# Kernel optimization log

Measured on AMD Instinct MI355X. Metric: run time of the kernel, lower is better.

Reference implementation:

```python
import jax, jax.numpy as jnp
import numpy as np

N_NODES = 50000
N_EDGES = 800000
C_IN = 128
C_OUT = 128
K = 6


def setup_inputs() -> dict:
    key = jax.random.key(0)
    ks = jax.random.split(key, 8)
    nodes = jax.random.normal(ks[0], (N_NODES, C_IN), dtype=jnp.float32)
    edges = jax.random.uniform(ks[1], (N_EDGES,), dtype=jnp.float32)
    senders = jax.random.randint(ks[2], (N_EDGES,), 0, N_NODES, dtype=jnp.int32)
    receivers = jax.random.randint(ks[3], (N_EDGES,), 0, N_NODES, dtype=jnp.int32)
    # K independent Dense(out_channels) layers (kernel + bias each), plus extra module bias
    W = jax.random.normal(ks[4], (K, C_IN, C_OUT), dtype=jnp.float32) / jnp.sqrt(jnp.float32(C_IN))
    b_dense = jax.random.normal(ks[5], (K, C_OUT), dtype=jnp.float32) * 0.01
    bias = jnp.zeros((C_OUT,), dtype=jnp.float32)
    return {"nodes": nodes, "edges": edges, "senders": senders, "receivers": receivers,
            "W": W, "b_dense": b_dense, "bias": bias}


def reference(nodes, edges, senders, receivers, W, b_dense, bias):
    n = nodes.shape[0]
    # Laplacian L = D - A with A[s, r] = w. deg_i = sum of weights of edges with sender i.
    deg = jax.ops.segment_sum(edges, senders, num_segments=n)
    # lambda_max = 2 * max(L.data) where L.data = concat(deg, -edges)
    lambda_max = 2.0 * jnp.maximum(deg.max(), (-edges).max())
    scale = 2.0 / lambda_max  # L_hat = (2/lambda_max) * L

    def Lmatvec(x):  # (2L/lambda_max) @ x via gather + segment_sum
        agg = jax.ops.segment_sum(edges[:, None] * x[receivers], senders, num_segments=n)
        return scale * (deg[:, None] * x - agg)

    Tx0 = nodes
    out = Tx0 @ W[0] + b_dense[0]
    Tx1 = Lmatvec(Tx0)
    out = out + Tx1 @ W[1] + b_dense[1]
    for k in range(2, K):
        Tx2 = 2.0 * Lmatvec(Tx1) - Tx0
        out = out + Tx2 @ W[k] + b_dense[k]
        Tx0, Tx1 = Tx1, Tx2
    return out + bias
```

## Files before the change

### kernel.cpp

```cpp
#include <hip/hip_runtime.h>
#include <hip/hip_fp16.h>

#define C 128
#define KORD 6
#define KD (KORD * C)
#define EPB 2048

typedef __attribute__((ext_vector_type(8))) short short8;
typedef __attribute__((ext_vector_type(4))) float f32x4;

__device__ __forceinline__ short f2bf(float f) {
  unsigned u = __float_as_uint(f);
  unsigned r = (u + 0x7fffu + ((u >> 16) & 1u)) >> 16;
  return (short)r;
}
__device__ __forceinline__ float bf2f(short s) {
  return __uint_as_float(((unsigned)(unsigned short)s) << 16);
}

__device__ __forceinline__ unsigned enc_f32(float f) {
  unsigned u = __float_as_uint(f);
  return (u & 0x80000000u) ? ~u : (u | 0x80000000u);
}
__device__ __forceinline__ float dec_f32(unsigned u) {
  return (u & 0x80000000u) ? __uint_as_float(u ^ 0x80000000u) : __uint_as_float(~u);
}

__global__ void prep_kernel(const float* __restrict__ W, const float* __restrict__ bd,
                            const float* __restrict__ bias, short* __restrict__ Wt,
                            float* __restrict__ bsum, const float* __restrict__ nodes,
                            short* __restrict__ xb, int n) {
  int i = blockIdx.x * blockDim.x + threadIdx.x;
  if (i < KD * C) {
    int k = i >> 7, nn = i & 127;
    Wt[(size_t)nn * KD + k] = f2bf(W[i]);
  }
  if (i < C) {
    float s = bias[i];
#pragma unroll
    for (int k = 0; k < KORD; ++k) s += bd[k * C + i];
    bsum[i] = s;
  }
  if (i < n * 32) {
    int row = i >> 5, c4 = i & 31;
    float4 v = ((const float4*)nodes)[(size_t)row * 32 + c4];
    short4 o;
    o.x = f2bf(v.x); o.y = f2bf(v.y); o.z = f2bf(v.z); o.w = f2bf(v.w);
    ((short4*)(xb + (size_t)row * KD))[c4] = o;
  }
}

__global__ __launch_bounds__(256) void p1_count_kernel(const int* __restrict__ senders,
                                                       const float* __restrict__ edges, int ne,
                                                       int* __restrict__ hist, int NB,
                                                       unsigned* __restrict__ umax) {
  __shared__ int h[256];
  int t = threadIdx.x;
  h[t] = 0;
  __syncthreads();
  int base = blockIdx.x * EPB;
  int end = min(base + EPB, ne);
  float m = -INFINITY;
  for (int i = base + t; i < end; i += 256) {
    atomicAdd(&h[senders[i] >> 8], 1);
    m = fmaxf(m, -edges[i]);
  }
#pragma unroll
  for (int off = 32; off > 0; off >>= 1) m = fmaxf(m, __shfl_down(m, off, 64));
  if ((t & 63) == 0) atomicMax(umax, enc_f32(m));
  __syncthreads();
  hist[t * NB + blockIdx.x] = h[t];
}

__global__ __launch_bounds__(1024) void scan1_kernel(const int* __restrict__ counts,
                                                     int* __restrict__ offsets,
                                                     int* __restrict__ bsums, int n) {
  int t = threadIdx.x;
  int i = blockIdx.x * 1024 + t;
  int lane = t & 63, w = t >> 6;
  int v = (i < n) ? counts[i] : 0;
  int s = v;
#pragma unroll
  for (int d = 1; d < 64; d <<= 1) {
    int o = __shfl_up(s, d, 64);
    if (lane >= d) s += o;
  }
  __shared__ int wsum[16];
  if (lane == 63) wsum[w] = s;
  __syncthreads();
  if (t < 16) {
    int ws = wsum[t];
#pragma unroll
    for (int d = 1; d < 16; d <<= 1) {
      int o = __shfl_up(ws, d, 64);
      if (t >= d) ws += o;
    }
    wsum[t] = ws;
  }
  __syncthreads();
  int excl = s - v + (w > 0 ? wsum[w - 1] : 0);
  if (i < n) offsets[i] = excl;
  if (t == 1023) bsums[blockIdx.x] = wsum[15];
}

__global__ __launch_bounds__(1024) void scan2_kernel(int* __restrict__ bsums, int nb) {
  int t = threadIdx.x;
  int lane = t & 63, w = t >> 6;
  int v = (t < nb) ? bsums[t] : 0;
  int s = v;
#pragma unroll
  for (int d = 1; d < 64; d <<= 1) {
    int o = __shfl_up(s, d, 64);
    if (lane >= d) s += o;
  }
  __shared__ int wsum[16];
  if (lane == 63) wsum[w] = s;
  __syncthreads();
  if (t < 16) {
    int ws = wsum[t];
#pragma unroll
    for (int d = 1; d < 16; d <<= 1) {
      int o = __shfl_up(ws, d, 64);
      if (t >= d) ws += o;
    }
    wsum[t] = ws;
  }
  __syncthreads();
  int excl = s - v + (w > 0 ? wsum[w - 1] : 0);
  if (t < nb) bsums[t] = excl;
}

__global__ __launch_bounds__(256) void p1_scatter_kernel(
    const int* __restrict__ senders, const int* __restrict__ receivers,
    const float* __restrict__ edges, int ne, const int* __restrict__ scanned,
    const int* __restrict__ bsums, int NB, int2* __restrict__ bkt) {
  __shared__ int basec[256];
  int t = threadIdx.x;
  int idx = t * NB + blockIdx.x;
  basec[t] = scanned[idx] + bsums[idx >> 10];
  __syncthreads();
  int base = blockIdx.x * EPB;
  int end = min(base + EPB, ne);
  for (int i = base + t; i < end; i += 256) {
    int s = senders[i];
    int pos = atomicAdd(&basec[s >> 8], 1);
    int2 rec;
    rec.x = __float_as_int(edges[i]);
    rec.y = receivers[i] | ((s & 255) << 16);
    bkt[pos] = rec;
  }
}

__global__ __launch_bounds__(256) void p2_finalize_kernel(
    const int2* __restrict__ bkt, const int* __restrict__ scanned,
    const int* __restrict__ bsums, int NB, int NBUCK, int ne, int n,
    unsigned* __restrict__ csr_wr, int* __restrict__ offsets, float* __restrict__ degf,
    unsigned* __restrict__ umax, int* __restrict__ ticket, float* __restrict__ scalep) {
  __shared__ int h[256];
  __shared__ int cur[256];
  __shared__ float dg[256];
  __shared__ int wsum[4];
  __shared__ float wmax[4];
  int t = threadIdx.x;
  int b = blockIdx.x;
  int i0 = b * NB;
  int base = scanned[i0] + bsums[i0 >> 10];
  int bend = ne;
  if (b != NBUCK - 1) {
    int i1 = (b + 1) * NB;
    bend = scanned[i1] + bsums[i1 >> 10];
  }
  h[t] = 0;
  dg[t] = 0.f;
  __syncthreads();
  for (int i = base + t; i < bend; i += 256) atomicAdd(&h[(bkt[i].y >> 16) & 255], 1);
  __syncthreads();
  int lane = t & 63, w = t >> 6;
  int v = h[t];
  int s = v;
#pragma unroll
  for (int d = 1; d < 64; d <<= 1) {
    int o = __shfl_up(s, d, 64);
    if (lane >= d) s += o;
  }
  if (lane == 63) wsum[w] = s;
  __syncthreads();
  int carry = 0;
#pragma unroll
  for (int j = 0; j < 4; ++j) carry += (j < w) ? wsum[j] : 0;
  int excl = s - v + carry;
  int node = b * 256 + t;
  if (node < n) offsets[node] = base + excl;
  cur[t] = base + excl;
  __syncthreads();
  for (int i = base + t; i < bend; i += 256) {
    int2 rec = bkt[i];
    int bin = (rec.y >> 16) & 255;
    int pos = atomicAdd(&cur[bin], 1);
    __half hh = __float2half(__int_as_float(rec.x));
    csr_wr[pos] = (unsigned)(rec.y & 0xFFFF) | ((unsigned)__half_as_ushort(hh) << 16);
    atomicAdd(&dg[bin], __half2float(hh));
  }
  __syncthreads();
  float d = dg[t];
  if (node < n) degf[node] = d;
  float m = (node < n) ? d : 0.f;
#pragma unroll
  for (int off = 32; off > 0; off >>= 1) m = fmaxf(m, __shfl_down(m, off, 64));
  if (lane == 0) wmax[w] = m;
  __syncthreads();
  if (t == 0) {
    float mm = fmaxf(fmaxf(wmax[0], wmax[1]), fmaxf(wmax[2], wmax[3]));
    atomicMax(umax, enc_f32(mm));
    if (b == NBUCK - 1) offsets[n] = ne;
    __threadfence();
    int done = atomicAdd(ticket, 1);
    if (done == NBUCK - 1) {
      unsigned cu = atomicMax(umax, 0u);
      scalep[0] = 1.0f / dec_f32(cu);
    }
  }
}

__global__ __launch_bounds__(256, 8) void matvec_kernel(
    const short* __restrict__ xg,
    const short* __restrict__ zg,
    short* __restrict__ yg,
    const float* __restrict__ deg, const int* __restrict__ offsets,
    const unsigned* __restrict__ csr_wr, const float* __restrict__ scalep, float coef, int n) {
  int wid = (blockIdx.x * blockDim.x + threadIdx.x) >> 6;
  int lane = threadIdx.x & 63;
  int sub = lane & 15;
  int quarter = lane >> 4;
  if (wid >= n) return;
  float sc = scalep[0] * coef;
  int e0 = offsets[wid], e1 = offsets[wid + 1];
  float d = 0.f;
  short8 xo, zv;
  if (quarter == 0) {
    d = deg[wid];
    xo = *(const short8*)(xg + (size_t)wid * KD + sub * 8);
    if (zg) zv = *(const short8*)(zg + (size_t)wid * KD + sub * 8);
  }
  float a[8];
#pragma unroll
  for (int j = 0; j < 8; ++j) a[j] = 0.f;
  int elast = e1 - 1;
  const short* xs = xg + sub * 8;
  for (int e = e0 + quarter; e < e1; e += 16) {
    int eb1 = e + 4, eb2 = e + 8, eb3 = e + 12;
    unsigned p0 = csr_wr[e];
    unsigned p1 = csr_wr[min(eb1, elast)];
    unsigned p2 = csr_wr[min(eb2, elast)];
    unsigned p3 = csr_wr[min(eb3, elast)];
    short8 v0 = *(const short8*)(xs + (p0 & 0xFFFFu) * KD);
    short8 v1 = *(const short8*)(xs + (p1 & 0xFFFFu) * KD);
    short8 v2 = *(const short8*)(xs + (p2 & 0xFFFFu) * KD);
    short8 v3 = *(const short8*)(xs + (p3 & 0xFFFFu) * KD);
    float w0 = __half2float(__ushort_as_half((unsigned short)(p0 >> 16)));
    float w1 = (eb1 < e1) ? __half2float(__ushort_as_half((unsigned short)(p1 >> 16))) : 0.f;
    float w2 = (eb2 < e1) ? __half2float(__ushort_as_half((unsigned short)(p2 >> 16))) : 0.f;
    float w3 = (eb3 < e1) ? __half2float(__ushort_as_half((unsigned short)(p3 >> 16))) : 0.f;
#pragma unroll
    for (int j = 0; j < 8; ++j) {
      float t0 = fmaf(w0, bf2f(v0[j]), a[j]);
      float t1 = fmaf(w1, bf2f(v1[j]), t0);
      float t2 = fmaf(w2, bf2f(v2[j]), t1);
      a[j] = fmaf(w3, bf2f(v3[j]), t2);
    }
  }
#pragma unroll
  for (int j = 0; j < 8; ++j) {
    a[j] += __shfl_xor(a[j], 16, 64);
    a[j] += __shfl_xor(a[j], 32, 64);
  }
  if (quarter == 0) {
    float r[8];
#pragma unroll
    for (int j = 0; j < 8; ++j) r[j] = sc * fmaf(d, bf2f(xo[j]), -a[j]);
    if (zg) {
#pragma unroll
      for (int j = 0; j < 8; ++j) r[j] -= bf2f(zv[j]);
    }
    short8 o;
#pragma unroll
    for (int j = 0; j < 8; ++j) o[j] = f2bf(r[j]);
    *(short8*)(yg + (size_t)wid * KD + sub * 8) = o;
  }
}

#define BK 64
#define LDP (BK + 8)
__global__ __launch_bounds__(256) void mfma_gemm_kernel(const short* __restrict__ Xb,
                                                        const short* __restrict__ Wt,
                                                        const float* __restrict__ bsum,
                                                        float* __restrict__ out, int n) {
  __shared__ short Al[64 * LDP];
  __shared__ short Bl[128 * LDP];
  int t = threadIdx.x;
  int w = t >> 6, lane = t & 63;
  int m = lane & 15, q = lane >> 4;
  int row0 = blockIdx.x * 64;
  int c0 = w * 32;

  f32x4 acc[4][2];
#pragma unroll
  for (int i = 0; i < 4; ++i)
#pragma unroll
    for (int j = 0; j < 2; ++j) acc[i][j] = (f32x4){0.f, 0.f, 0.f, 0.f};

  for (int k0 = 0; k0 < KD; k0 += BK) {
    __syncthreads();
#pragma unroll
    for (int p = 0; p < 2; ++p) {
      int idx = t + 256 * p;
      int r = idx >> 3, u = idx & 7;
      int gr = min(row0 + r, n - 1);
      short8 v = *(const short8*)(Xb + (size_t)gr * KD + k0 + u * 8);
      *(short8*)(Al + r * LDP + u * 8) = v;
    }
#pragma unroll
    for (int p = 0; p < 4; ++p) {
      int idx = t + 256 * p;
      int cc = idx >> 3, u = idx & 7;
      short8 v = *(const short8*)(Wt + (size_t)cc * KD + k0 + u * 8);
      *(short8*)(Bl + cc * LDP + u * 8) = v;
    }
    __syncthreads();
#pragma unroll
    for (int s = 0; s < 2; ++s) {
      int ko = s * 32 + q * 8;
      short8 b0 = *(const short8*)(Bl + (c0 + m) * LDP + ko);
      short8 b1 = *(const short8*)(Bl + (c0 + 16 + m) * LDP + ko);
#pragma unroll
      for (int rt = 0; rt < 4; ++rt) {
        short8 av = *(const short8*)(Al + (rt * 16 + m) * LDP + ko);
        acc[rt][0] = __builtin_amdgcn_mfma_f32_16x16x32_bf16(av, b0, acc[rt][0], 0, 0, 0);
        acc[rt][1] = __builtin_amdgcn_mfma_f32_16x16x32_bf16(av, b1, acc[rt][1], 0, 0, 0);
      }
    }
  }

#pragma unroll
  for (int ct = 0; ct < 2; ++ct) {
    int col = c0 + ct * 16 + m;
    float bs = bsum[col];
#pragma unroll
    for (int rt = 0; rt < 4; ++rt) {
#pragma unroll
      for (int i = 0; i < 4; ++i) {
        int row = row0 + rt * 16 + q * 4 + i;
        if (row < n) out[(size_t)row * C + col] = acc[rt][ct][i] + bs;
      }
    }
  }
}

extern "C" void kernel_launch(void* const* d_in, const int* in_sizes, int n_in,
                              void* d_out, int out_size, void* d_ws, size_t ws_size,
                              hipStream_t stream) {
  const float* nodes = (const float*)d_in[0];
  const float* edges = (const float*)d_in[1];
  const int* senders = (const int*)d_in[2];
  const int* receivers = (const int*)d_in[3];
  const float* W = (const float*)d_in[4];
  const float* b_dense = (const float*)d_in[5];
  const float* bias = (const float*)d_in[6];
  float* out = (float*)d_out;
  int n = in_sizes[0] / C;
  int ne = in_sizes[1];
  int NB = (ne + EPB - 1) / EPB;
  int NBUCK = (n + 255) >> 8;
  int M = 256 * NB;
  int nb2 = (M + 1023) / 1024;

  char* ws = (char*)d_ws;
  size_t off = 0;
  auto alloc = [&](size_t b) { size_t r = off; off += (b + 255) & ~(size_t)255; return r; };
  float* degf = (float*)(ws + alloc((size_t)n * 4));
  int* offsets = (int*)(ws + alloc((size_t)(n + 1) * 4));
  int* hist = (int*)(ws + alloc((size_t)M * 4));
  int* bsums = (int*)(ws + alloc((size_t)nb2 * 4));
  int2* bkt = (int2*)(ws + alloc((size_t)ne * 8));
  unsigned* csr_wr = (unsigned*)(ws + alloc((size_t)ne * 4));
  unsigned* umax = (unsigned*)(ws + alloc(8));
  float* scalep = (float*)(ws + alloc(4));
  float* bsum = (float*)(ws + alloc(C * 4));
  short* Xb = (short*)(ws + alloc((size_t)n * KD * 2));
  short* Wt = (short*)(ws + alloc((size_t)KD * C * 2));
  (void)ws_size; (void)n_in; (void)out_size;

  hipMemsetAsync(umax, 0, 8, stream);

  int prep_n = max(KD * C, n * 32);
  prep_kernel<<<(prep_n + 255) / 256, 256, 0, stream>>>(W, b_dense, bias, Wt, bsum, nodes, Xb, n);

  p1_count_kernel<<<NB, 256, 0, stream>>>(senders, edges, ne, hist, NB, umax);
  scan1_kernel<<<nb2, 1024, 0, stream>>>(hist, hist, bsums, M);
  scan2_kernel<<<1, 1024, 0, stream>>>(bsums, nb2);
  p1_scatter_kernel<<<NB, 256, 0, stream>>>(senders, receivers, edges, ne, hist, bsums, NB, bkt);
  p2_finalize_kernel<<<NBUCK, 256, 0, stream>>>(bkt, hist, bsums, NB, NBUCK, ne, n, csr_wr,
                                                offsets, degf, umax, (int*)(umax + 1), scalep);

  int mvblocks = (n * 64 + 255) / 256;

  matvec_kernel<<<mvblocks, 256, 0, stream>>>(Xb + 0 * C, nullptr, Xb + 1 * C,
                                              degf, offsets, csr_wr, scalep, 1.0f, n);
  matvec_kernel<<<mvblocks, 256, 0, stream>>>(Xb + 1 * C, Xb + 0 * C, Xb + 2 * C,
                                              degf, offsets, csr_wr, scalep, 2.0f, n);
  matvec_kernel<<<mvblocks, 256, 0, stream>>>(Xb + 2 * C, Xb + 1 * C, Xb + 3 * C,
                                              degf, offsets, csr_wr, scalep, 2.0f, n);
  matvec_kernel<<<mvblocks, 256, 0, stream>>>(Xb + 3 * C, Xb + 2 * C, Xb + 4 * C,
                                              degf, offsets, csr_wr, scalep, 2.0f, n);
  matvec_kernel<<<mvblocks, 256, 0, stream>>>(Xb + 4 * C, Xb + 3 * C, Xb + 5 * C,
                                              degf, offsets, csr_wr, scalep, 2.0f, n);

  mfma_gemm_kernel<<<(n + 63) / 64, 256, 0, stream>>>(Xb, Wt, bsum, out, n);
}
```

Baseline: 324.8 us.

## Split node feature buffers into 64-channel halves processed by separate matvec blocks

Stores the Chebyshev feature stack as planar 64-channel halves, each n×64 bf16, instead of interleaved rows of 768 channels. Each matvec launch now covers both halves with twice as many blocks, each wave gathering 128-byte rows for eight edges at a time. The GEMM A-tile loads and the prep conversion are updated to match. The aim is better cache locality for the random neighbour gathers, since each half's working set is smaller, at the cost of reading the CSR indices twice. It also folds the umax memset into the prep kernel.

```diff
diff --git a/kernel.cpp b/kernel.cpp
--- a/kernel.cpp
+++ b/kernel.cpp
@@ -26,11 +26,16 @@
   return (u & 0x80000000u) ? __uint_as_float(u ^ 0x80000000u) : __uint_as_float(~u);
 }
 
+
 __global__ void prep_kernel(const float* __restrict__ W, const float* __restrict__ bd,
                             const float* __restrict__ bias, short* __restrict__ Wt,
                             float* __restrict__ bsum, const float* __restrict__ nodes,
-                            short* __restrict__ xb, int n) {
+                            short* __restrict__ xb, int n, unsigned* __restrict__ umax) {
   int i = blockIdx.x * blockDim.x + threadIdx.x;
+  if (i == 0) {
+    umax[0] = 0u;
+    umax[1] = 0u;
+  }
   if (i < KD * C) {
     int k = i >> 7, nn = i & 127;
     Wt[(size_t)nn * KD + k] = f2bf(W[i]);
@@ -46,7 +51,9 @@
     float4 v = ((const float4*)nodes)[(size_t)row * 32 + c4];
     short4 o;
     o.x = f2bf(v.x); o.y = f2bf(v.y); o.z = f2bf(v.z); o.w = f2bf(v.w);
-    ((short4*)(xb + (size_t)row * KD))[c4] = o;
+    int h = c4 >> 4;
+    int cc = c4 & 15;
+    ((short4*)(xb + (size_t)h * ((size_t)n * 64) + (size_t)row * 64))[cc] = o;
   }
 }
 
@@ -223,58 +230,59 @@
 }
 
 __global__ __launch_bounds__(256, 8) void matvec_kernel(
-    const short* __restrict__ xg,
-    const short* __restrict__ zg,
-    short* __restrict__ yg,
+    const short* __restrict__ xh,
+    const short* __restrict__ zh,
+    short* __restrict__ yh,
     const float* __restrict__ deg, const int* __restrict__ offsets,
-    const unsigned* __restrict__ csr_wr, const float* __restrict__ scalep, float coef, int n) {
-  int wid = (blockIdx.x * blockDim.x + threadIdx.x) >> 6;
+    const unsigned* __restrict__ csr_wr, const float* __restrict__ scalep,
+    float coef, int n, int pblocks) {
+  int b = blockIdx.x;
+  int h = (b >= pblocks) ? 1 : 0;
+  int wid = ((b - h * pblocks) * 256 + threadIdx.x) >> 6;
+  if (wid >= n) return;
   int lane = threadIdx.x & 63;
-  int sub = lane & 15;
-  int quarter = lane >> 4;
-  if (wid >= n) return;
+  int g = lane >> 3;
+  int sub = lane & 7;
+  size_t n64 = (size_t)n * 64;
+  const short* xg = xh + (size_t)h * n64;
+  const short* zg = zh ? zh + (size_t)h * n64 : (const short*)0;
+  short* yg = yh + (size_t)h * n64;
   float sc = scalep[0] * coef;
   int e0 = offsets[wid], e1 = offsets[wid + 1];
   float d = 0.f;
-  short8 xo, zv;
-  if (quarter == 0) {
+  short8 xo = {0, 0, 0, 0, 0, 0, 0, 0};
+  short8 zv = {0, 0, 0, 0, 0, 0, 0, 0};
+  if (g == 0) {
     d = deg[wid];
-    xo = *(const short8*)(xg + (size_t)wid * KD + sub * 8);
-    if (zg) zv = *(const short8*)(zg + (size_t)wid * KD + sub * 8);
+    xo = *(const short8*)(xg + (size_t)wid * 64 + sub * 8);
+    if (zg) zv = *(const short8*)(zg + (size_t)wid * 64 + sub * 8);
   }
   float a[8];
 #pragma unroll
   for (int j = 0; j < 8; ++j) a[j] = 0.f;
   int elast = e1 - 1;
   const short* xs = xg + sub * 8;
-  for (int e = e0 + quarter; e < e1; e += 16) {
-    int eb1 = e + 4, eb2 = e + 8, eb3 = e + 12;
+  for (int e = e0 + g; e < e1; e += 16) {
+    int e2 = e + 8;
     unsigned p0 = csr_wr[e];
-    unsigned p1 = csr_wr[min(eb1, elast)];
-    unsigned p2 = csr_wr[min(eb2, elast)];
-    unsigned p3 = csr_wr[min(eb3, elast)];
-    short8 v0 = *(const short8*)(xs + (p0 & 0xFFFFu) * KD);
-    short8 v1 = *(const short8*)(xs + (p1 & 0xFFFFu) * KD);
-    short8 v2 = *(const short8*)(xs + (p2 & 0xFFFFu) * KD);
-    short8 v3 = *(const short8*)(xs + (p3 & 0xFFFFu) * KD);
+    unsigned p1 = csr_wr[min(e2, elast)];
+    short8 v0 = *(const short8*)(xs + (p0 & 0xFFFFu) * 64);
+    short8 v1 = *(const short8*)(xs + (p1 & 0xFFFFu) * 64);
     float w0 = __half2float(__ushort_as_half((unsigned short)(p0 >> 16)));
-    float w1 = (eb1 < e1) ? __half2float(__ushort_as_half((unsigned short)(p1 >> 16))) : 0.f;
-    float w2 = (eb2 < e1) ? __half2float(__ushort_as_half((unsigned short)(p2 >> 16))) : 0.f;
-    float w3 = (eb3 < e1) ? __half2float(__ushort_as_half((unsigned short)(p3 >> 16))) : 0.f;
+    float w1 = (e2 < e1) ? __half2float(__ushort_as_half((unsigned short)(p1 >> 16))) : 0.f;
 #pragma unroll
     for (int j = 0; j < 8; ++j) {
       float t0 = fmaf(w0, bf2f(v0[j]), a[j]);
-      float t1 = fmaf(w1, bf2f(v1[j]), t0);
-      float t2 = fmaf(w2, bf2f(v2[j]), t1);
-      a[j] = fmaf(w3, bf2f(v3[j]), t2);
+      a[j] = fmaf(w1, bf2f(v1[j]), t0);
     }
   }
 #pragma unroll
   for (int j = 0; j < 8; ++j) {
+    a[j] += __shfl_xor(a[j], 8, 64);
     a[j] += __shfl_xor(a[j], 16, 64);
     a[j] += __shfl_xor(a[j], 32, 64);
   }
-  if (quarter == 0) {
+  if (g == 0) {
     float r[8];
 #pragma unroll
     for (int j = 0; j < 8; ++j) r[j] = sc * fmaf(d, bf2f(xo[j]), -a[j]);
@@ -285,7 +293,7 @@
     short8 o;
 #pragma unroll
     for (int j = 0; j < 8; ++j) o[j] = f2bf(r[j]);
-    *(short8*)(yg + (size_t)wid * KD + sub * 8) = o;
+    *(short8*)(yg + (size_t)wid * 64 + sub * 8) = o;
   }
 }
 
@@ -302,6 +310,7 @@
   int m = lane & 15, q = lane >> 4;
   int row0 = blockIdx.x * 64;
   int c0 = w * 32;
+  size_t n64 = (size_t)n * 64;
 
   f32x4 acc[4][2];
 #pragma unroll
@@ -310,13 +319,14 @@
     for (int j = 0; j < 2; ++j) acc[i][j] = (f32x4){0.f, 0.f, 0.f, 0.f};
 
   for (int k0 = 0; k0 < KD; k0 += BK) {
+    const short* Ab = Xb + (size_t)(k0 >> 6) * n64;
     __syncthreads();
 #pragma unroll
     for (int p = 0; p < 2; ++p) {
       int idx = t + 256 * p;
       int r = idx >> 3, u = idx & 7;
       int gr = min(row0 + r, n - 1);
-      short8 v = *(const short8*)(Xb + (size_t)gr * KD + k0 + u * 8);
+      short8 v = *(const short8*)(Ab + (size_t)gr * 64 + u * 8);
       *(short8*)(Al + r * LDP + u * 8) = v;
     }
 #pragma unroll
@@ -382,7 +392,7 @@
   int* hist = (int*)(ws + alloc((size_t)M * 4));
   int* bsums = (int*)(ws + alloc((size_t)nb2 * 4));
   int2* bkt = (int2*)(ws + alloc((size_t)ne * 8));
-  unsigned* csr_wr = (unsigned*)(ws + alloc((size_t)ne * 4));
+  unsigned* csr = (unsigned*)(ws + alloc((size_t)ne * 4));
   unsigned* umax = (unsigned*)(ws + alloc(8));
   float* scalep = (float*)(ws + alloc(4));
   float* bsum = (float*)(ws + alloc(C * 4));
@@ -390,30 +400,29 @@
   short* Wt = (short*)(ws + alloc((size_t)KD * C * 2));
   (void)ws_size; (void)n_in; (void)out_size;
 
-  hipMemsetAsync(umax, 0, 8, stream);
+  size_t n64 = (size_t)n * 64;
 
   int prep_n = max(KD * C, n * 32);
-  prep_kernel<<<(prep_n + 255) / 256, 256, 0, stream>>>(W, b_dense, bias, Wt, bsum, nodes, Xb, n);
+  prep_kernel<<<(prep_n + 255) / 256, 256, 0, stream>>>(W, b_dense, bias, Wt, bsum, nodes,
+                                                        Xb, n, umax);
 
   p1_count_kernel<<<NB, 256, 0, stream>>>(senders, edges, ne, hist, NB, umax);
   scan1_kernel<<<nb2, 1024, 0, stream>>>(hist, hist, bsums, M);
   scan2_kernel<<<1, 1024, 0, stream>>>(bsums, nb2);
   p1_scatter_kernel<<<NB, 256, 0, stream>>>(senders, receivers, edges, ne, hist, bsums, NB, bkt);
-  p2_finalize_kernel<<<NBUCK, 256, 0, stream>>>(bkt, hist, bsums, NB, NBUCK, ne, n, csr_wr,
+  p2_finalize_kernel<<<NBUCK, 256, 0, stream>>>(bkt, hist, bsums, NB, NBUCK, ne, n, csr,
                                                 offsets, degf, umax, (int*)(umax + 1), scalep);
 
-  int mvblocks = (n * 64 + 255) / 256;
-
-  matvec_kernel<<<mvblocks, 256, 0, stream>>>(Xb + 0 * C, nullptr, Xb + 1 * C,
-                                              degf, offsets, csr_wr, scalep, 1.0f, n);
-  matvec_kernel<<<mvblocks, 256, 0, stream>>>(Xb + 1 * C, Xb + 0 * C, Xb + 2 * C,
-                                              degf, offsets, csr_wr, scalep, 2.0f, n);
-  matvec_kernel<<<mvblocks, 256, 0, stream>>>(Xb + 2 * C, Xb + 1 * C, Xb + 3 * C,
-                                              degf, offsets, csr_wr, scalep, 2.0f, n);
-  matvec_kernel<<<mvblocks, 256, 0, stream>>>(Xb + 3 * C, Xb + 2 * C, Xb + 4 * C,
-                                              degf, offsets, csr_wr, scalep, 2.0f, n);
-  matvec_kernel<<<mvblocks, 256, 0, stream>>>(Xb + 4 * C, Xb + 3 * C, Xb + 5 * C,
-                                              degf, offsets, csr_wr, scalep, 2.0f, n);
+  int pblocks = (n * 64 + 255) / 256;
+  int mvblocks = 2 * pblocks;
+
+  for (int r = 0; r < 5; ++r) {
+    const short* xh = Xb + (size_t)(2 * r) * n64;
+    const short* zh = (r == 0) ? (const short*)nullptr : Xb + (size_t)(2 * (r - 1)) * n64;
+    short* yh = Xb + (size_t)(2 * (r + 1)) * n64;
+    matvec_kernel<<<mvblocks, 256, 0, stream>>>(xh, zh, yh, degf, offsets, csr, scalep,
+                                                (r == 0) ? 1.0f : 2.0f, n, pblocks);
+  }
 
   mfma_gemm_kernel<<<(n + 63) / 64, 256, 0, stream>>>(Xb, Wt, bsum, out, n);
 }
```

New measurement: 366.3 us. 1.13x slower.
